# Kernel tuning notes

Measured on AMD Instinct MI355X. Metric: run time of the kernel, lower is better.

## Reference

```python
import jax, jax.numpy as jnp
from jax import lax
import numpy as np

B, T = 16, 96      # sentences per batch, EDUs per document
K = 64             # kcluster
D = 768            # BERT_DIM
H = 400            # n_lstm_hidden
L = 3              # n_lstm_layers
M = 500            # n_mlp_arc
NEG = -1e9


def setup_inputs() -> dict:
    key = jax.random.key(0)
    ks = jax.random.split(key, 16)
    s = 0.1
    return {
        "embed_table": jax.random.normal(ks[0], (K, D), jnp.float32) * s,
        "multinomial": jax.random.normal(ks[1], (K, K), jnp.float32) * s,
        "wih0": jax.random.normal(ks[2], (2, 4 * H, D), jnp.float32) * s,
        "wih": jax.random.normal(ks[3], (L - 1, 2, 4 * H, 2 * H), jnp.float32) * s,
        "whh": jax.random.normal(ks[4], (L, 2, 4 * H, H), jnp.float32) * s,
        "b": jax.random.normal(ks[5], (L, 2, 4 * H), jnp.float32) * s,
        "mlp_h_w": jax.random.normal(ks[6], (M, 2 * H), jnp.float32) * s,
        "mlp_h_b": jax.random.normal(ks[7], (M,), jnp.float32) * s,
        "mlp_d_w": jax.random.normal(ks[8], (M, 2 * H), jnp.float32) * s,
        "mlp_d_b": jax.random.normal(ks[9], (M,), jnp.float32) * s,
        "biaffine_w": jax.random.normal(ks[10], (M, M), jnp.float32) * s,
        "kmeans_labels": jax.random.randint(ks[11], (B, T), 0, K),
        "heads": jax.random.randint(ks[12], (B, T - 1), 0, T),
    }


def _lse(x, axis):
    m = jnp.max(x, axis=axis, keepdims=True)
    return jnp.squeeze(m, axis) + jnp.log(jnp.sum(jnp.exp(x - m), axis=axis))


def _lstm_dir(x, Wih, Whh, bias, reverse):
    # x: [B, T, in] -> [B, T, H]; torch gate order i,f,g,o; bias = b_ih + b_hh
    xs = jnp.swapaxes(x, 0, 1)

    def step(carry, xt):
        h, c = carry
        g = xt @ Wih.T + h @ Whh.T + bias
        i, f, gg, o = jnp.split(g, 4, axis=-1)
        c = jax.nn.sigmoid(f) * c + jax.nn.sigmoid(i) * jnp.tanh(gg)
        h = jax.nn.sigmoid(o) * jnp.tanh(c)
        return (h, c), h

    z = jnp.zeros((x.shape[0], Whh.shape[1]), x.dtype)
    _, hs = lax.scan(step, (z, z), xs, reverse=reverse)
    return jnp.swapaxes(hs, 0, 1)


def _inside(s):
    # Eisner first-order inside algorithm in the log semiring.
    # s[h, d] = log-score of arc h -> d. Returns log-partition.
    n = s.shape[0]
    eye = jnp.eye(n, dtype=bool)
    C_r = jnp.where(eye, 0.0, NEG)  # complete, head on left
    C_l = jnp.where(eye, 0.0, NEG)  # complete, head on right
    I_r = jnp.full((n, n), NEG)
    I_l = jnp.full((n, n), NEG)
    for w in range(1, n):
        i = jnp.arange(n - w)
        j = i + w
        r = jnp.arange(w)
        ii = i[:, None]
        # incomplete spans: split k in [i, j-1]
        inc = _lse(C_r[ii, ii + r] + C_l[ii + r + 1, j[:, None]], axis=1)
        I_r = I_r.at[i, j].set(inc + s[i, j])
        I_l = I_l.at[i, j].set(inc + s[j, i])
        # complete right: split k in [i+1, j]
        rr = jnp.arange(1, w + 1)
        cr = _lse(I_r[ii, ii + rr] + C_r[ii + rr, j[:, None]], axis=1)
        C_r = C_r.at[i, j].set(cr)
        # complete left: split k in [i, j-1]
        cl = _lse(C_l[ii, ii + r] + I_l[ii + r, j[:, None]], axis=1)
        C_l = C_l.at[i, j].set(cl)
    return C_r[0, n - 1]


def reference(embed_table, multinomial, wih0, wih, whh, b, mlp_h_w, mlp_h_b,
              mlp_d_w, mlp_d_b, biaffine_w, kmeans_labels, heads):
    # embed lookup of kmeans cluster labels (word_embed=False branch)
    x = embed_table[kmeans_labels]  # [B, T, D]
    # 3-layer BiLSTM (eval mode: dropout = identity)
    for l in range(L):
        Wf = wih0[0] if l == 0 else wih[l - 1, 0]
        Wb = wih0[1] if l == 0 else wih[l - 1, 1]
        hf = _lstm_dir(x, Wf, whh[l, 0], b[l, 0], reverse=False)
        hb = _lstm_dir(x, Wb, whh[l, 1], b[l, 1], reverse=True)
        x = jnp.concatenate([hf, hb], axis=-1)  # [B, T, 2H]
    # arc MLPs (LeakyReLU(0.1) as in the biaffine parser MLP)
    arc_h = jax.nn.leaky_relu(x @ mlp_h_w.T + mlp_h_b, 0.1)
    arc_d = jax.nn.leaky_relu(x @ mlp_d_w.T + mlp_d_b, 0.1)
    # biaffine arc scores: s_arc[b, dep, head]
    s_arc = jnp.einsum('bxi,ij,byj->bxy', arc_d, biaffine_w, arc_h)
    # encoder_p[b, head, dep] = log_softmax over heads, then permute(0,2,1)
    p = jnp.swapaxes(jax.nn.log_softmax(s_arc, axis=-1), 1, 2)
    # reconstruction weight from raw multinomial over cluster labels
    rec = multinomial[kmeans_labels[:, :, None], kmeans_labels[:, None, :]]
    joint = p + rec  # [B, T, T]
    # score of the given (gold) tree: heads[b, d-1] -> d for deps 1..T-1
    deps = jnp.arange(1, T)
    best_score = joint[jnp.arange(B)[:, None], heads, deps[None, :]].sum(axis=1)
    # Eisner log-partition per sentence over encoder_p
    partition = jax.vmap(_inside)(p)
    # supervised loss: mean of -(best_score - partition)
    return jnp.mean(partition - best_score)
```

## Files before the change

kernel.cpp:

```cpp
#include <hip/hip_runtime.h>
#include <cmath>

#define DEV __device__ __forceinline__


#define NBLK_LSTM 400

DEV float wred_max(float v){ for(int o=32;o;o>>=1) v=fmaxf(v,__shfl_xor(v,o)); return v; }
DEV float wred_sum(float v){ for(int o=32;o;o>>=1) v+=__shfl_xor(v,o); return v; }
DEV float sigf(float x){ return 1.f/(1.f+__expf(-x)); }

DEV float agent_ld(const float* p){
  return __hip_atomic_load(p, __ATOMIC_RELAXED, __HIP_MEMORY_SCOPE_AGENT);
}
DEV void agent_st(float* p, float v){
  __hip_atomic_store(p, v, __ATOMIC_RELAXED, __HIP_MEMORY_SCOPE_AGENT);
}

__global__ __launch_bounds__(256) void g_gather(const float* __restrict__ Gtab,
                                                const int* __restrict__ labels,
                                                float* __restrict__ G){
  long idx = (long)blockIdx.x*256 + threadIdx.x;
  if (idx >= 1536L*800) return;
  int bt = (int)(idx / 800), d4 = (int)(idx - (long)bt*800);
  const float4* src = (const float4*)(Gtab + (size_t)labels[bt]*3200) + d4;
  ((float4*)(G + (size_t)bt*3200))[d4] = *src;
}

__global__ __launch_bounds__(256) void trans_sq(const float* __restrict__ w,
                                                float* __restrict__ wt){
  int idx = blockIdx.x*256 + threadIdx.x;
  if (idx >= 250000) return;
  int j = idx/500, i = idx%500;
  wt[idx] = w[(long)i*500 + j];
}

__global__ __launch_bounds__(256) void gemm_abt(const float* __restrict__ A,
                                                const float* __restrict__ Bm,
                                                float* __restrict__ C,
                                                const float* __restrict__ bias,
                                                int M, int N, int K,
                                                long sA, long sB, long sC, int leaky){
  A  += (long)blockIdx.z * sA;
  Bm += (long)blockIdx.z * sB;
  C  += (long)blockIdx.z * sC;
  __shared__ float As[16][68];
  __shared__ float Bs[16][68];
  int tid = threadIdx.x;
  int tx = tid & 15, ty = tid >> 4;
  int m0 = blockIdx.x * 64, n0 = blockIdx.y * 64;
  int lrow = tid >> 2, lc = (tid & 3) * 4;
  float acc[4][4] = {};
  for (int k0 = 0; k0 < K; k0 += 16) {
    #pragma unroll
    for (int u = 0; u < 4; u++) {
      int k = k0 + lc + u;
      int am = m0 + lrow;
      As[lc+u][lrow] = (am < M && k < K) ? A[(long)am*K + k] : 0.f;
      int bn = n0 + lrow;
      Bs[lc+u][lrow] = (bn < N && k < K) ? Bm[(long)bn*K + k] : 0.f;
    }
    __syncthreads();
    #pragma unroll
    for (int kk = 0; kk < 16; kk++) {
      float a[4], bb[4];
      #pragma unroll
      for (int u=0;u<4;u++){ a[u]=As[kk][ty*4+u]; bb[u]=Bs[kk][tx*4+u]; }
      #pragma unroll
      for (int i=0;i<4;i++)
        #pragma unroll
        for (int j=0;j<4;j++) acc[i][j] = fmaf(a[i], bb[j], acc[i][j]);
    }
    __syncthreads();
  }
  #pragma unroll
  for (int i=0;i<4;i++){
    int m = m0 + ty*4 + i;
    if (m >= M) continue;
    #pragma unroll
    for (int j=0;j<4;j++){
      int n = n0 + tx*4 + j;
      if (n >= N) continue;
      float v = acc[i][j];
      if (bias) v += bias[n];
      if (leaky) v = v > 0.f ? v : 0.1f*v;
      C[(long)m*N + n] = v;
    }
  }
}

__global__ __launch_bounds__(256) void mlp2_kern(const float* __restrict__ A,
                                                 const float* __restrict__ Wh,
                                                 const float* __restrict__ bh,
                                                 const float* __restrict__ Wd,
                                                 const float* __restrict__ bd,
                                                 float* __restrict__ Ch,
                                                 float* __restrict__ Cd){
  const float* Bm  = blockIdx.z ? Wd : Wh;
  const float* bias= blockIdx.z ? bd : bh;
  float* C         = blockIdx.z ? Cd : Ch;
  const int M = 1536, N = 500, K = 800;
  __shared__ float As[16][68];
  __shared__ float Bs[16][68];
  int tid = threadIdx.x;
  int tx = tid & 15, ty = tid >> 4;
  int m0 = blockIdx.x * 64, n0 = blockIdx.y * 64;
  int lrow = tid >> 2, lc = (tid & 3) * 4;
  float acc[4][4] = {};
  for (int k0 = 0; k0 < K; k0 += 16) {
    #pragma unroll
    for (int u = 0; u < 4; u++) {
      int k = k0 + lc + u;
      As[lc+u][lrow] = A[(long)(m0+lrow)*K + k];
      int bn = n0 + lrow;
      Bs[lc+u][lrow] = (bn < N) ? Bm[(long)bn*K + k] : 0.f;
    }
    __syncthreads();
    #pragma unroll
    for (int kk = 0; kk < 16; kk++) {
      float a[4], bb[4];
      #pragma unroll
      for (int u=0;u<4;u++){ a[u]=As[kk][ty*4+u]; bb[u]=Bs[kk][tx*4+u]; }
      #pragma unroll
      for (int i=0;i<4;i++)
        #pragma unroll
        for (int j=0;j<4;j++) acc[i][j] = fmaf(a[i], bb[j], acc[i][j]);
    }
    __syncthreads();
  }
  #pragma unroll
  for (int i=0;i<4;i++){
    int m = m0 + ty*4 + i;
    #pragma unroll
    for (int j=0;j<4;j++){
      int n = n0 + tx*4 + j;
      if (n >= N) continue;
      float v = acc[i][j] + bias[n];
      v = v > 0.f ? v : 0.1f*v;
      C[(long)m*N + n] = v;
    }
  }
}

__global__ __launch_bounds__(256) void gemm128(const float* __restrict__ A,
                                               const float* __restrict__ Bm,
                                               float* __restrict__ C,
                                               const float* __restrict__ bias,
                                               int M, int N, int K, int leaky){
  __shared__ float As[16][132];
  __shared__ float Bs[16][132];
  int tid = threadIdx.x;
  int tx = tid & 15, ty = tid >> 4;
  int m0 = blockIdx.x*128, n0 = blockIdx.y*128;
  int lr = tid >> 1, lq = (tid & 1)*8;
  const float* Arow = A + (size_t)(m0+lr)*K + lq;
  const float* Brow = Bm + (size_t)(n0+lr)*K + lq;
  bool bok = (n0 + lr) < N;
  float acc[8][8] = {};
  for (int k0 = 0; k0 < K; k0 += 16){
    if (k0 + 16 <= K){
      float4 a0 = *(const float4*)(Arow + k0);
      float4 a1 = *(const float4*)(Arow + k0 + 4);
      float4 b0 = {0,0,0,0}, b1 = {0,0,0,0};
      if (bok){ b0 = *(const float4*)(Brow + k0); b1 = *(const float4*)(Brow + k0 + 4); }
      As[lq+0][lr]=a0.x; As[lq+1][lr]=a0.y; As[lq+2][lr]=a0.z; As[lq+3][lr]=a0.w;
      As[lq+4][lr]=a1.x; As[lq+5][lr]=a1.y; As[lq+6][lr]=a1.z; As[lq+7][lr]=a1.w;
      Bs[lq+0][lr]=b0.x; Bs[lq+1][lr]=b0.y; Bs[lq+2][lr]=b0.z; Bs[lq+3][lr]=b0.w;
      Bs[lq+4][lr]=b1.x; Bs[lq+5][lr]=b1.y; Bs[lq+6][lr]=b1.z; Bs[lq+7][lr]=b1.w;
    } else {
      #pragma unroll
      for (int u = 0; u < 8; u++){
        int k = k0 + lq + u;
        As[lq+u][lr] = (k < K) ? Arow[k0+u] : 0.f;
        Bs[lq+u][lr] = (bok && k < K) ? Brow[k0+u] : 0.f;
      }
    }
    __syncthreads();
    #pragma unroll
    for (int kk = 0; kk < 16; kk++){
      float4 a0 = *(const float4*)&As[kk][ty*8];
      float4 a1 = *(const float4*)&As[kk][ty*8+4];
      float4 b0 = *(const float4*)&Bs[kk][tx*8];
      float4 b1 = *(const float4*)&Bs[kk][tx*8+4];
      float av[8] = {a0.x,a0.y,a0.z,a0.w,a1.x,a1.y,a1.z,a1.w};
      float bv[8] = {b0.x,b0.y,b0.z,b0.w,b1.x,b1.y,b1.z,b1.w};
      #pragma unroll
      for (int i=0;i<8;i++)
        #pragma unroll
        for (int j=0;j<8;j++) acc[i][j] = fmaf(av[i], bv[j], acc[i][j]);
    }
    __syncthreads();
  }
  bool full = (n0 + 128 <= N);
  #pragma unroll
  for (int i = 0; i < 8; i++){
    int m = m0 + ty*8 + i;
    float* Crow = C + (size_t)m*N;
    if (full){
      float4 v0, v1;
      float* p0 = &v0.x; float* p1 = &v1.x;
      #pragma unroll
      for (int j = 0; j < 4; j++){
        int n = n0 + tx*8 + j;
        float v = acc[i][j];
        if (bias) v += bias[n];
        if (leaky) v = v > 0.f ? v : 0.1f*v;
        p0[j] = v;
      }
      #pragma unroll
      for (int j = 4; j < 8; j++){
        int n = n0 + tx*8 + j;
        float v = acc[i][j];
        if (bias) v += bias[n];
        if (leaky) v = v > 0.f ? v : 0.1f*v;
        p1[j-4] = v;
      }
      *(float4*)(Crow + n0 + tx*8)     = v0;
      *(float4*)(Crow + n0 + tx*8 + 4) = v1;
    } else {
      #pragma unroll
      for (int j = 0; j < 8; j++){
        int n = n0 + tx*8 + j;
        if (n < N){
          float v = acc[i][j];
          if (bias) v += bias[n];
          if (leaky) v = v > 0.f ? v : 0.1f*v;
          Crow[n] = v;
        }
      }
    }
  }
}

__global__ __launch_bounds__(128) void lstm_grid(const float* __restrict__ G,
                                                 const float* __restrict__ whh,
                                                 float* __restrict__ xout,
                                                 float* __restrict__ hbufG,
                                                 unsigned* __restrict__ flags,
                                                 int layer){
  __shared__ float Wl[32*404];
  __shared__ float hl[4*404];
  __shared__ float gb[32][5];
  int tid = threadIdx.x;
  int bid = blockIdx.x;
  int dir     = bid / 200;
  int quarter = (bid / 50) % 4;
  int slice   = bid % 50;
  int jj0  = slice * 8;
  int bat0 = quarter * 4;
  int fbase = dir*200 + quarter*50;
  const float* whhL = whh + (size_t)(layer*2 + dir)*1600*400;
  for (int i = tid; i < 3200; i += 128){
    int r = i/100, k4 = i%100;
    int g = r>>3, jjr = r&7;
    float4 v = *(const float4*)(whhL + (size_t)(g*400 + jj0 + jjr)*400 + k4*4);
    *(float4*)&Wl[r*404 + k4*4] = v;
  }
  for (int i = tid; i < 4*404; i += 128) hl[i] = 0.f;
  int ks   = (tid>>2)&15;
  int rowg = (tid&3) | ((tid>>6)<<2);
  const float* hb = hl;
  const float* wb = Wl + rowg*4*404;
  int ebl = (tid>>3)&3;
  int ejj = tid & 7;
  int ebat = bat0 + ebl;
  const float* gbase = G + (size_t)ebat*96*3200 + dir*1600 + jj0 + ejj;
  float* xo = xout + (size_t)ebat*96*800 + dir*400 + jj0 + ejj;
  float c = 0.f;
  float g0=0.f, g1=0.f, g2=0.f, g3=0.f;
  if (tid < 32){
    const float* gp0 = gbase + (size_t)(dir ? 95 : 0)*3200;
    g0 = gp0[0]; g1 = gp0[400]; g2 = gp0[800]; g3 = gp0[1200];
  }
  __syncthreads();
  for (int s = 0; s < 96; s++){
    int t = dir ? 95 - s : s;
    float acc[4][4] = {};
    #pragma unroll
    for (int q = 0; q < 6; ++q){
      int k4 = q*16 + ks;
      float4 h0 = *(const float4*)&hb[0*404 + k4*4];
      float4 h1 = *(const float4*)&hb[1*404 + k4*4];
      float4 h2 = *(const float4*)&hb[2*404 + k4*4];
      float4 h3 = *(const float4*)&hb[3*404 + k4*4];
      float4 w0 = *(const float4*)&wb[0*404 + k4*4];
      float4 w1 = *(const float4*)&wb[1*404 + k4*4];
      float4 w2 = *(const float4*)&wb[2*404 + k4*4];
      float4 w3 = *(const float4*)&wb[3*404 + k4*4];
      #pragma unroll
      for (int bi=0; bi<4; bi++){
        float4 hq = bi==0?h0: bi==1?h1: bi==2?h2: h3;
        #pragma unroll
        for (int ri=0; ri<4; ri++){
          float4 wq = ri==0?w0: ri==1?w1: ri==2?w2: w3;
          acc[bi][ri] = fmaf(hq.x,wq.x, fmaf(hq.y,wq.y,
                        fmaf(hq.z,wq.z, fmaf(hq.w,wq.w, acc[bi][ri]))));
        }
      }
    }
    if (ks < 4){
      int k4 = 96 + ks;
      float4 h0 = *(const float4*)&hb[0*404 + k4*4];
      float4 h1 = *(const float4*)&hb[1*404 + k4*4];
      float4 h2 = *(const float4*)&hb[2*404 + k4*4];
      float4 h3 = *(const float4*)&hb[3*404 + k4*4];
      float4 w0 = *(const float4*)&wb[0*404 + k4*4];
      float4 w1 = *(const float4*)&wb[1*404 + k4*4];
      float4 w2 = *(const float4*)&wb[2*404 + k4*4];
      float4 w3 = *(const float4*)&wb[3*404 + k4*4];
      #pragma unroll
      for (int bi=0; bi<4; bi++){
        float4 hq = bi==0?h0: bi==1?h1: bi==2?h2: h3;
        #pragma unroll
        for (int ri=0; ri<4; ri++){
          float4 wq = ri==0?w0: ri==1?w1: ri==2?w2: w3;
          acc[bi][ri] = fmaf(hq.x,wq.x, fmaf(hq.y,wq.y,
                        fmaf(hq.z,wq.z, fmaf(hq.w,wq.w, acc[bi][ri]))));
        }
      }
    }
    #pragma unroll
    for (int bi=0; bi<4; bi++)
      #pragma unroll
      for (int ri=0; ri<4; ri++){
        float v = acc[bi][ri];
        v += __shfl_xor(v, 4);
        v += __shfl_xor(v, 8);
        v += __shfl_xor(v, 16);
        v += __shfl_xor(v, 32);
        acc[bi][ri] = v;
      }
    if (ks == 0){
      #pragma unroll
      for (int ri=0; ri<4; ri++)
        #pragma unroll
        for (int bi=0; bi<4; bi++)
          gb[rowg*4+ri][bi] = acc[bi][ri];
    }
    __syncthreads();
    int par = s & 1;
    if (tid < 32){
      float ai = gb[     ejj][ebl] + g0;
      float af = gb[ 8 + ejj][ebl] + g1;
      float ag = gb[16 + ejj][ebl] + g2;
      float ao = gb[24 + ejj][ebl] + g3;
      c = sigf(af)*c + sigf(ai)*tanhf(ag);
      float hv = sigf(ao)*tanhf(c);
      agent_st(&hbufG[((size_t)(par*2 + dir)*16 + ebat)*400 + jj0 + ejj], hv);
      xo[(size_t)t*800] = hv;
    }
    if (s < 95){
      unsigned target = (unsigned)(layer*95 + s + 1);
      __syncthreads();
      if (tid == 0)
        __hip_atomic_store(&flags[bid*16], target, __ATOMIC_RELAXED,
                           __HIP_MEMORY_SCOPE_AGENT);
      if (tid < 32){
        int tn = dir ? 94 - s : s + 1;
        const float* gp = gbase + (size_t)tn*3200;
        g0 = gp[0]; g1 = gp[400]; g2 = gp[800]; g3 = gp[1200];
      }
      if (tid < 50){
        while (__hip_atomic_load(&flags[(fbase + tid)*16], __ATOMIC_RELAXED,
                                 __HIP_MEMORY_SCOPE_AGENT) < target){
          __builtin_amdgcn_s_sleep(1);
        }
      }
      __syncthreads();
      const float* hsrc = hbufG + (size_t)(par*2 + dir)*6400 + bat0*400;
      float hA[4], hB[4], hC[4], hT;
      #pragma unroll
      for (int bat = 0; bat < 4; bat++){
        hA[bat] = agent_ld(hsrc + bat*400 + tid);
        hB[bat] = agent_ld(hsrc + bat*400 + 128 + tid);
        hC[bat] = agent_ld(hsrc + bat*400 + 256 + tid);
      }
      hT = (tid < 64) ? agent_ld(hsrc + (tid>>4)*400 + 384 + (tid&15)) : 0.f;
      #pragma unroll
      for (int bat = 0; bat < 4; bat++){
        hl[bat*404 + tid]       = hA[bat];
        hl[bat*404 + 128 + tid] = hB[bat];
        hl[bat*404 + 256 + tid] = hC[bat];
      }
      if (tid < 64) hl[(tid>>4)*404 + 384 + (tid&15)] = hT;
      __syncthreads();
    }
  }
}

__global__ __launch_bounds__(256) void softmax_p(const float* __restrict__ sarc,
                                                 float* __restrict__ p){
  int row  = blockIdx.x*4 + (threadIdx.x >> 6);
  int lane = threadIdx.x & 63;
  int b = row/96, x = row%96;
  const float* s = sarc + (long)(b*96 + x)*96;
  float v1 = s[lane];
  float v2 = (lane+64 < 96) ? s[lane+64] : -INFINITY;
  float mx = wred_max(fmaxf(v1,v2));
  float sm = wred_sum(__expf(v1-mx) + __expf(v2-mx));
  float lse = mx + __logf(sm);
  float* pr = p + (long)b*9216;
  pr[lane*96 + x] = v1 - lse;
  if (lane+64 < 96) pr[(lane+64)*96 + x] = v2 - lse;
}

__global__ __launch_bounds__(128) void best_kern(const float* __restrict__ p,
                                                 const float* __restrict__ multinomial,
                                                 const int* __restrict__ labels,
                                                 const int* __restrict__ heads,
                                                 float* __restrict__ best){
  int b = blockIdx.x, tid = threadIdx.x;
  float acc = 0.f;
  for (int ti = tid; ti < 95; ti += 128) {
    int y = heads[b*95 + ti];
    int x = ti + 1;
    acc += p[(long)b*9216 + y*96 + x]
         + multinomial[(long)labels[b*96 + y]*64 + labels[b*96 + x]];
  }
  acc = wred_sum(acc);
  __shared__ float tmp[2];
  if ((tid & 63) == 0) tmp[tid >> 6] = acc;
  __syncthreads();
  if (tid == 0) best[b] = tmp[0] + tmp[1];
}

__global__ __launch_bounds__(1024) void inside_kern(const float* __restrict__ p,
                                                    float* __restrict__ part){
  __shared__ float Cp[96][97];
  __shared__ float Ipp[96][97];
  __shared__ float Xp[96][97];
  __shared__ float Pl[96][97];
  int b = blockIdx.x;
  const float* pB = p + (long)b*9216;
  int tid = threadIdx.x;
  for (int idx = tid; idx < 96*97; idx += 1024) {
    int row = idx/97, col = idx%97;
    float d = (row == col) ? 0.f : -1e9f;
    Cp[row][col] = d;
    Xp[row][col] = d;
    Ipp[row][col] = -1e9f;
  }
  for (int idx = tid; idx < 9216; idx += 1024)
    Pl[idx/96][idx%96] = pB[idx];
  __syncthreads();
  int g = tid >> 3, l = tid & 7;
  for (int w = 1; w < 96; w++){
    int n = 96 - w;
    if (g < n){
      int i = g, j = i + w;
      {
        const float* pa  = &Cp[i][i];
        const float* pb2 = &Cp[j][i+1];
        float vb[12]; float m = -1e30f;
        #pragma unroll
        for (int k = 0; k < 12; k++){
          vb[k] = -1e30f;
          if (k*8 < w){
            int r = l + k*8;
            if (r < w){ float v = pa[r] + pb2[r]; vb[k] = v; m = fmaxf(m, v); }
          }
        }
        m = fmaxf(m, __shfl_xor(m,1));
        m = fmaxf(m, __shfl_xor(m,2));
        m = fmaxf(m, __shfl_xor(m,4));
        float s = 0.f;
        #pragma unroll
        for (int k = 0; k < 12; k++){
          if (k*8 < w) s += __expf(vb[k] - m);
        }
        s += __shfl_xor(s,1); s += __shfl_xor(s,2); s += __shfl_xor(s,4);
        float inc = m + __logf(s);
        if (l == 0){
          Ipp[i][j] = inc + Pl[i][j];
          Ipp[j][i] = inc + Pl[j][i];
        }
      }
      {
        const float* pa1 = &Ipp[i][i+1];
        const float* pb1 = &Xp[j][i+1];
        const float* pa2 = &Xp[i][i];
        const float* pb2 = &Ipp[j][i];
        float v1b[12], v2b[12]; float m1 = -1e30f, m2 = -1e30f;
        #pragma unroll
        for (int k = 0; k < 12; k++){
          v1b[k] = -1e30f; v2b[k] = -1e30f;
          if (k*8 < w){
            int r = l + k*8;
            if (r < w){
              float v1 = pa1[r] + pb1[r]; v1b[k] = v1; m1 = fmaxf(m1, v1);
              float v2 = pa2[r] + pb2[r]; v2b[k] = v2; m2 = fmaxf(m2, v2);
            }
          }
        }
        m1 = fmaxf(m1, __shfl_xor(m1,1));
        m1 = fmaxf(m1, __shfl_xor(m1,2));
        m1 = fmaxf(m1, __shfl_xor(m1,4));
        m2 = fmaxf(m2, __shfl_xor(m2,1));
        m2 = fmaxf(m2, __shfl_xor(m2,2));
        m2 = fmaxf(m2, __shfl_xor(m2,4));
        float s1 = 0.f, s2 = 0.f;
        #pragma unroll
        for (int k = 0; k < 12; k++){
          if (k*8 < w){ s1 += __expf(v1b[k] - m1); s2 += __expf(v2b[k] - m2); }
        }
        s1 += __shfl_xor(s1,1); s1 += __shfl_xor(s1,2); s1 += __shfl_xor(s1,4);
        s2 += __shfl_xor(s2,1); s2 += __shfl_xor(s2,2); s2 += __shfl_xor(s2,4);
        if (l == 0){
          float cr = m1 + __logf(s1);
          float cl = m2 + __logf(s2);
          Cp[i][j] = cr; Xp[j][i] = cr;
          Cp[j][i] = cl; Xp[i][j] = cl;
        }
      }
    }
    __syncthreads();
  }
  if (tid == 0) part[b] = Cp[0][95];
}

__global__ __launch_bounds__(64) void final_kern(const float* __restrict__ part,
                                                 const float* __restrict__ best,
                                                 float* __restrict__ out){
  int lane = threadIdx.x;
  float v = (lane < 16) ? part[lane] - best[lane] : 0.f;
  v = wred_sum(v);
  if (lane == 0) out[0] = v * (1.f/16.f);
}

extern "C" void kernel_launch(void* const* d_in, const int* in_sizes, int n_in,
                              void* d_out, int out_size, void* d_ws, size_t ws_size,
                              hipStream_t stream) {
  const float* emb   = (const float*)d_in[0];
  const float* multi = (const float*)d_in[1];
  const float* wih0  = (const float*)d_in[2];
  const float* wih   = (const float*)d_in[3];
  const float* whh   = (const float*)d_in[4];
  const float* bias  = (const float*)d_in[5];
  const float* mhw   = (const float*)d_in[6];
  const float* mhb   = (const float*)d_in[7];
  const float* mdw   = (const float*)d_in[8];
  const float* mdb   = (const float*)d_in[9];
  const float* biaf  = (const float*)d_in[10];
  const int*   labels= (const int*)d_in[11];
  const int*   heads = (const int*)d_in[12];
  float* out = (float*)d_out;

  float* ws = (float*)d_ws;
  size_t off = 0;
  auto alloc = [&](size_t n){ float* q = ws + off; off += n; return q; };
  float* G    = alloc(1536L*3200);
  float* Gtab = alloc(64L*3200);
  float* xA   = alloc(1536L*800);
  float* xB   = alloc(1536L*800);
  float* WTb  = alloc(500L*500);
  float* arcH = alloc(1536L*500);
  float* arcD = alloc(1536L*500);
  float* tmp  = alloc(1536L*500);
  float* sarc = alloc(16L*96*96);
  float* pbuf = alloc(16L*96*96);
  float* hbufG= alloc(2L*2*16*400);
  unsigned* flags = (unsigned*)alloc(NBLK_LSTM*16);
  float* part = alloc(16);
  float* best = alloc(16);
  (void)ws_size; (void)in_sizes; (void)n_in; (void)out_size;

  hipMemsetAsync(flags, 0, NBLK_LSTM*16*sizeof(unsigned), stream);

  trans_sq<<<(250000+255)/256, 256, 0, stream>>>(biaf, WTb);

  gemm_abt<<<dim3(1,50), 256, 0, stream>>>(emb, wih0, Gtab, bias,
                                           64, 3200, 768, 0,0,0, 0);
  g_gather<<<4800, 256, 0, stream>>>(Gtab, labels, G);
  lstm_grid<<<NBLK_LSTM, 128, 0, stream>>>(G, whh, xA, hbufG, flags, 0);

  const float* xin = xA;
  float* xout = xB;
  for (int l = 1; l < 3; l++) {
    const float* W = wih + (size_t)(l-1)*2*1600*800;
    gemm128<<<dim3(12,25), 256, 0, stream>>>(xin, W, G, bias + l*3200,
                                             1536, 3200, 800, 0);
    lstm_grid<<<NBLK_LSTM, 128, 0, stream>>>(G, whh, xout, hbufG, flags, l);
    xin = xout;
    xout = (l==1) ? xA : xB;
  }
  mlp2_kern<<<dim3(24,8,2), 256, 0, stream>>>(xin, mhw, mhb, mdw, mdb, arcH, arcD);
  dim3 gm(24, 8, 1);
  gemm_abt<<<gm, 256, 0, stream>>>(arcD, WTb, tmp, nullptr, 1536, 500, 500, 0,0,0, 0);
  dim3 gs(2, 2, 16);
  gemm_abt<<<gs, 256, 0, stream>>>(tmp, arcH, sarc, nullptr, 96, 96, 500,
                                   96L*500, 96L*500, 96L*96, 0);
  softmax_p<<<384, 256, 0, stream>>>(sarc, pbuf);
  best_kern<<<16, 128, 0, stream>>>(pbuf, multi, labels, heads, best);
  inside_kern<<<16, 1024, 0, stream>>>(pbuf, part);
  final_kern<<<1, 64, 0, stream>>>(part, best, out);
}
```

Measured before the change: 1.970 ms.

## Drop biaffine transpose kernel, fuse gold-score into inside kernel, trim LSTM step sync

Result: no change. 1.963 ms (-0.4%).

```diff
diff --git a/kernel.cpp b/kernel.cpp
--- a/kernel.cpp
+++ b/kernel.cpp
@@ -25,14 +25,6 @@
   int bt = (int)(idx / 800), d4 = (int)(idx - (long)bt*800);
   const float4* src = (const float4*)(Gtab + (size_t)labels[bt]*3200) + d4;
   ((float4*)(G + (size_t)bt*3200))[d4] = *src;
-}
-
-__global__ __launch_bounds__(256) void trans_sq(const float* __restrict__ w,
-                                                float* __restrict__ wt){
-  int idx = blockIdx.x*256 + threadIdx.x;
-  if (idx >= 250000) return;
-  int j = idx/500, i = idx%500;
-  wt[idx] = w[(long)i*500 + j];
 }
 
 __global__ __launch_bounds__(256) void gemm_abt(const float* __restrict__ A,
@@ -85,6 +77,52 @@
       if (bias) v += bias[n];
       if (leaky) v = v > 0.f ? v : 0.1f*v;
       C[(long)m*N + n] = v;
+    }
+  }
+}
+
+__global__ __launch_bounds__(256) void gemm_abn(const float* __restrict__ A,
+                                                const float* __restrict__ Bn,
+                                                float* __restrict__ C,
+                                                int M, int N, int K){
+  __shared__ float As[16][68];
+  __shared__ float Bs[16][68];
+  int tid = threadIdx.x;
+  int tx = tid & 15, ty = tid >> 4;
+  int m0 = blockIdx.x * 64, n0 = blockIdx.y * 64;
+  int lrow = tid >> 2, lc = (tid & 3) * 4;
+  float acc[4][4] = {};
+  for (int k0 = 0; k0 < K; k0 += 16) {
+    #pragma unroll
+    for (int u = 0; u < 4; u++) {
+      int k = k0 + lc + u;
+      int am = m0 + lrow;
+      As[lc+u][lrow] = (am < M && k < K) ? A[(long)am*K + k] : 0.f;
+      int bn = n0 + lrow;
+      Bs[lc+u][lrow] = (bn < N && k < K) ? Bn[(long)k*N + bn] : 0.f;
+    }
+    __syncthreads();
+    #pragma unroll
+    for (int kk = 0; kk < 16; kk++) {
+      float a[4], bb[4];
+      #pragma unroll
+      for (int u=0;u<4;u++){ a[u]=As[kk][ty*4+u]; bb[u]=Bs[kk][tx*4+u]; }
+      #pragma unroll
+      for (int i=0;i<4;i++)
+        #pragma unroll
+        for (int j=0;j<4;j++) acc[i][j] = fmaf(a[i], bb[j], acc[i][j]);
+    }
+    __syncthreads();
+  }
+  #pragma unroll
+  for (int i=0;i<4;i++){
+    int m = m0 + ty*4 + i;
+    if (m >= M) continue;
+    #pragma unroll
+    for (int j=0;j<4;j++){
+      int n = n0 + tx*4 + j;
+      if (n >= N) continue;
+      C[(long)m*N + n] = acc[i][j];
     }
   }
 }
@@ -339,23 +377,27 @@
     }
     __syncthreads();
     int par = s & 1;
+    float hv = 0.f;
     if (tid < 32){
       float ai = gb[     ejj][ebl] + g0;
       float af = gb[ 8 + ejj][ebl] + g1;
       float ag = gb[16 + ejj][ebl] + g2;
       float ao = gb[24 + ejj][ebl] + g3;
       c = sigf(af)*c + sigf(ai)*tanhf(ag);
-      float hv = sigf(ao)*tanhf(c);
-      agent_st(&hbufG[((size_t)(par*2 + dir)*16 + ebat)*400 + jj0 + ejj], hv);
-      xo[(size_t)t*800] = hv;
+      hv = sigf(ao)*tanhf(c);
+      if (s < 95)
+        agent_st(&hbufG[((size_t)(par*2 + dir)*16 + ebat)*400 + jj0 + ejj], hv);
     }
     if (s < 95){
       unsigned target = (unsigned)(layer*95 + s + 1);
-      __syncthreads();
-      if (tid == 0)
-        __hip_atomic_store(&flags[bid*16], target, __ATOMIC_RELAXED,
-                           __HIP_MEMORY_SCOPE_AGENT);
+      if (tid < 64){
+        asm volatile("s_waitcnt vmcnt(0)" ::: "memory");
+        if (tid == 0)
+          __hip_atomic_store(&flags[bid*16], target, __ATOMIC_RELAXED,
+                             __HIP_MEMORY_SCOPE_AGENT);
+      }
       if (tid < 32){
+        xo[(size_t)t*800] = hv;
         int tn = dir ? 94 - s : s + 1;
         const float* gp = gbase + (size_t)tn*3200;
         g0 = gp[0]; g1 = gp[400]; g2 = gp[800]; g3 = gp[1200];
@@ -384,6 +426,8 @@
       }
       if (tid < 64) hl[(tid>>4)*404 + 384 + (tid&15)] = hT;
       __syncthreads();
+    } else {
+      if (tid < 32) xo[(size_t)t*800] = hv;
     }
   }
 }
@@ -404,32 +448,17 @@
   if (lane+64 < 96) pr[(lane+64)*96 + x] = v2 - lse;
 }
 
-__global__ __launch_bounds__(128) void best_kern(const float* __restrict__ p,
-                                                 const float* __restrict__ multinomial,
-                                                 const int* __restrict__ labels,
-                                                 const int* __restrict__ heads,
-                                                 float* __restrict__ best){
-  int b = blockIdx.x, tid = threadIdx.x;
-  float acc = 0.f;
-  for (int ti = tid; ti < 95; ti += 128) {
-    int y = heads[b*95 + ti];
-    int x = ti + 1;
-    acc += p[(long)b*9216 + y*96 + x]
-         + multinomial[(long)labels[b*96 + y]*64 + labels[b*96 + x]];
-  }
-  acc = wred_sum(acc);
-  __shared__ float tmp[2];
-  if ((tid & 63) == 0) tmp[tid >> 6] = acc;
-  __syncthreads();
-  if (tid == 0) best[b] = tmp[0] + tmp[1];
-}
-
 __global__ __launch_bounds__(1024) void inside_kern(const float* __restrict__ p,
-                                                    float* __restrict__ part){
+                                                    const float* __restrict__ multinomial,
+                                                    const int* __restrict__ labels,
+                                                    const int* __restrict__ heads,
+                                                    float* __restrict__ part,
+                                                    float* __restrict__ best){
   __shared__ float Cp[96][97];
   __shared__ float Ipp[96][97];
   __shared__ float Xp[96][97];
   __shared__ float Pl[96][97];
+  __shared__ float bpart[16];
   int b = blockIdx.x;
   const float* pB = p + (long)b*9216;
   int tid = threadIdx.x;
@@ -443,6 +472,19 @@
   for (int idx = tid; idx < 9216; idx += 1024)
     Pl[idx/96][idx%96] = pB[idx];
   __syncthreads();
+  {
+    float accb = 0.f;
+    if (tid < 95){
+      int y = heads[b*95 + tid];
+      int x = tid + 1;
+      accb = Pl[y][x]
+           + multinomial[(long)labels[b*96 + y]*64 + labels[b*96 + x]];
+    }
+    accb = wred_sum(accb);
+    if ((tid & 63) == 0) bpart[tid >> 6] = accb;
+    __syncthreads();
+    if (tid == 0) best[b] = bpart[0] + bpart[1];
+  }
   int g = tid >> 3, l = tid & 7;
   for (int w = 1; w < 96; w++){
     int n = 96 - w;
@@ -552,7 +594,6 @@
   float* Gtab = alloc(64L*3200);
   float* xA   = alloc(1536L*800);
   float* xB   = alloc(1536L*800);
-  float* WTb  = alloc(500L*500);
   float* arcH = alloc(1536L*500);
   float* arcD = alloc(1536L*500);
   float* tmp  = alloc(1536L*500);
@@ -566,8 +607,6 @@
 
   hipMemsetAsync(flags, 0, NBLK_LSTM*16*sizeof(unsigned), stream);
 
-  trans_sq<<<(250000+255)/256, 256, 0, stream>>>(biaf, WTb);
-
   gemm_abt<<<dim3(1,50), 256, 0, stream>>>(emb, wih0, Gtab, bias,
                                            64, 3200, 768, 0,0,0, 0);
   g_gather<<<4800, 256, 0, stream>>>(Gtab, labels, G);
@@ -584,13 +623,11 @@
     xout = (l==1) ? xA : xB;
   }
   mlp2_kern<<<dim3(24,8,2), 256, 0, stream>>>(xin, mhw, mhb, mdw, mdb, arcH, arcD);
-  dim3 gm(24, 8, 1);
-  gemm_abt<<<gm, 256, 0, stream>>>(arcD, WTb, tmp, nullptr, 1536, 500, 500, 0,0,0, 0);
+  gemm_abn<<<dim3(24,8), 256, 0, stream>>>(arcD, biaf, tmp, 1536, 500, 500);
   dim3 gs(2, 2, 16);
   gemm_abt<<<gs, 256, 0, stream>>>(tmp, arcH, sarc, nullptr, 96, 96, 500,
                                    96L*500, 96L*500, 96L*96, 0);
   softmax_p<<<384, 256, 0, stream>>>(sarc, pbuf);
-  best_kern<<<16, 128, 0, stream>>>(pbuf, multi, labels, heads, best);
-  inside_kern<<<16, 1024, 0, stream>>>(pbuf, part);
+  inside_kern<<<16, 1024, 0, stream>>>(pbuf, multi, labels, heads, part, best);
   final_kern<<<1, 64, 0, stream>>>(part, best, out);
 }
```
